# Optimization experiments

Measured on AMD Instinct MI355X. Metric: run time of the kernel, lower is better.

## Reference

```python
import jax, jax.numpy as jnp
import numpy as np

E = 256
H = 512
LN_EPS = 1e-5
NORM_EPS = 1e-12


def setup_inputs() -> dict:
    key = jax.random.key(0)
    ks = jax.random.split(key, 8)
    B, N, M = 8, 128, 128
    track_features = jax.random.normal(ks[0], (B, N, E), dtype=jnp.float32)
    det_features = jax.random.normal(ks[1], (B, M, E), dtype=jnp.float32)
    # MLP params (torch Linear default init style: uniform, but values irrelevant for correctness harness)
    lim1 = 1.0 / np.sqrt(3 * E)
    W1 = jax.random.uniform(ks[2], (3 * E, H), minval=-lim1, maxval=lim1, dtype=jnp.float32)
    b1 = jax.random.uniform(ks[3], (H,), minval=-lim1, maxval=lim1, dtype=jnp.float32)
    gamma = jnp.ones((H,), dtype=jnp.float32)
    beta = jnp.zeros((H,), dtype=jnp.float32)
    lim2 = 1.0 / np.sqrt(H)
    W2 = jax.random.uniform(ks[4], (H, 1), minval=-lim2, maxval=lim2, dtype=jnp.float32)
    b2 = jax.random.uniform(ks[5], (1,), minval=-lim2, maxval=lim2, dtype=jnp.float32)
    return {"track_features": track_features, "det_features": det_features,
            "W1": W1, "b1": b1, "gamma": gamma, "beta": beta, "W2": W2, "b2": b2}


def _l2_normalize(x):
    # F.normalize(x, dim=-1): x / max(||x||_2, eps)
    n = jnp.sqrt(jnp.sum(x * x, axis=-1, keepdims=True))
    return x / jnp.maximum(n, NORM_EPS)


def reference(track_features, det_features, W1, b1, gamma, beta, W2, b2):
    t = _l2_normalize(track_features)   # (B, N, E)
    d = _l2_normalize(det_features)     # (B, M, E)
    tb = t[:, :, None, :]               # (B, N, 1, E)
    db = d[:, None, :, :]               # (B, 1, M, E)
    B, N, _ = t.shape
    M = d.shape[1]
    diff = jnp.abs(tb - db)                                  # (B, N, M, E)
    pair = jnp.concatenate([jnp.broadcast_to(tb, (B, N, M, E)),
                            jnp.broadcast_to(db, (B, N, M, E)),
                            diff], axis=-1)                  # (B, N, M, 3E)
    h = jnp.einsum('bnme,eh->bnmh', pair, W1) + b1           # (B, N, M, H)
    mu = jnp.mean(h, axis=-1, keepdims=True)
    var = jnp.mean((h - mu) ** 2, axis=-1, keepdims=True)
    h = (h - mu) * jax.lax.rsqrt(var + LN_EPS) * gamma + beta
    h = h * jax.nn.sigmoid(h)                                # SiLU
    out = jnp.einsum('bnmh,ho->bnmo', h, W2)[..., 0] + b2[0]  # (B, N, M)
    return out
```

## Files before the change

kernel.cpp:

```cpp
#include <hip/hip_runtime.h>
#include <hip/hip_bf16.h>
#include <cstdint>

typedef __bf16 bf16x8 __attribute__((ext_vector_type(8)));
typedef float f32x4 __attribute__((ext_vector_type(4)));

#define E_DIM 256
#define H_DIM 512
#define TSTR 260

__global__ __launch_bounds__(256)
void w1conv_kernel(const float* __restrict__ W1, __bf16* __restrict__ W1cc) {
    int u = blockIdx.x * 256 + threadIdx.x;
    int j   = u & 3;
    int h   = (u >> 2) & 511;
    int c   = (u >> 11) & 7;
    int mat = u >> 14;
    bf16x8 v;
#pragma unroll
    for (int i = 0; i < 8; ++i)
        v[i] = (__bf16)W1[(size_t)(mat * 256 + c * 32 + j * 8 + i) * H_DIM + h];
    *(bf16x8*)(W1cc + ((size_t)(mat * 8 + c) * 512 + h) * 32 + j * 8) = v;
}

__global__ __launch_bounds__(512, 4)
void pq_mfma_kernel(const float* __restrict__ track, const float* __restrict__ det,
                    const __bf16* __restrict__ W1cc, const float* __restrict__ b1,
                    float* __restrict__ P, float* __restrict__ Q) {
    __shared__ __align__(16) __bf16 Ash[64 * 256];
    __shared__ float sclS[64];

    int tid  = threadIdx.x;
    int lane = tid & 63;
    int wave = tid >> 6;
    int lq   = lane >> 4;
    int lc   = lane & 15;

    int blk = blockIdx.x;
    bool isP = blk < 16;
    int r0 = (blk & 15) * 64;
    const float* src = isP ? track : det;

#pragma unroll
    for (int i = 0; i < 8; ++i) {
        int row = wave * 8 + i;
        float4 x = ((const float4*)(src + (size_t)(r0 + row) * E_DIM))[lane];
        float ss = x.x*x.x + x.y*x.y + x.z*x.z + x.w*x.w;
#pragma unroll
        for (int off = 32; off > 0; off >>= 1) ss += __shfl_xor(ss, off);
        if (lane == 0) sclS[row] = 1.0f / fmaxf(sqrtf(ss), 1e-12f);
    }
    __syncthreads();

#pragma unroll
    for (int r = 0; r < 4; ++r) {
        int row = r * 16 + lc;
        float st = sclS[row];
        const float* gp = src + (size_t)(r0 + row) * E_DIM + wave * 32 + lq * 8;
        float4 t0 = *(const float4*)gp;
        float4 t1 = *(const float4*)(gp + 4);
        bf16x8 v;
        v[0] = (__bf16)(t0.x * st); v[1] = (__bf16)(t0.y * st);
        v[2] = (__bf16)(t0.z * st); v[3] = (__bf16)(t0.w * st);
        v[4] = (__bf16)(t1.x * st); v[5] = (__bf16)(t1.y * st);
        v[6] = (__bf16)(t1.z * st); v[7] = (__bf16)(t1.w * st);
        *(bf16x8*)&Ash[(size_t)(r * 512 + wave * 64 + lane) * 8] = v;
    }
    __syncthreads();

    const uint4* Wg = (const uint4*)W1cc + (isP ? 0 : 16384);
    int hb = wave * 64 + lc;
    bf16x8 bwA[4], bwB[4];
#pragma unroll
    for (int ht = 0; ht < 4; ++ht)
        bwA[ht] = __builtin_bit_cast(bf16x8, Wg[(hb + ht * 16) * 4 + lq]);

    f32x4 acc[4][4];
#pragma unroll
    for (int pt = 0; pt < 4; ++pt)
#pragma unroll
        for (int ht = 0; ht < 4; ++ht)
            acc[pt][ht] = (f32x4){0.f, 0.f, 0.f, 0.f};

#pragma unroll
    for (int c = 0; c < 8; ++c) {
        bf16x8* cur = (c & 1) ? bwB : bwA;
        bf16x8* nxt = (c & 1) ? bwA : bwB;
        if (c < 7) {
#pragma unroll
            for (int ht = 0; ht < 4; ++ht)
                nxt[ht] = __builtin_bit_cast(bf16x8, Wg[(c + 1) * 2048 + (hb + ht * 16) * 4 + lq]);
        }
#pragma unroll
        for (int pt = 0; pt < 4; ++pt) {
            bf16x8 af = *(const bf16x8*)&Ash[(size_t)((pt * 8 + c) * 64 + lane) * 8];
#pragma unroll
            for (int ht = 0; ht < 4; ++ht)
                acc[pt][ht] = __builtin_amdgcn_mfma_f32_16x16x32_bf16(cur[ht], af, acc[pt][ht], 0, 0, 0);
        }
    }

    float* dst = isP ? P : Q;
#pragma unroll
    for (int ht = 0; ht < 4; ++ht) {
        int h = wave * 64 + ht * 16 + lq * 4;
        f32x4 bvv = (f32x4){0.f, 0.f, 0.f, 0.f};
        if (isP) bvv = *(const f32x4*)&b1[h];
#pragma unroll
        for (int pt = 0; pt < 4; ++pt) {
            f32x4 o = acc[pt][ht] + bvv;
            *(f32x4*)&dst[(size_t)(r0 + pt * 16 + lc) * H_DIM + h] = o;
        }
    }
}

__global__ __launch_bounds__(512, 4)
void main_kernel(const float* __restrict__ track, const float* __restrict__ det,
                 const __bf16* __restrict__ W1cc,
                 const float* __restrict__ P, const float* __restrict__ Q,
                 const float* __restrict__ gamma, const float* __restrict__ beta,
                 const float* __restrict__ W2, const float* __restrict__ b2,
                 float* __restrict__ out) {
    __shared__ __align__(16) char SMEM[49408];
    __bf16* Ash  = (__bf16*)SMEM;
    float*  tsl  = (float*)(SMEM + 32768);
    float*  dsl  = (float*)(SMEM + 41088);
    float*  LNr1 = (float*)(SMEM + 32768);
    float*  LNr2 = (float*)(SMEM + 35072);
    float*  Red2 = (float*)(SMEM + 37376);
    float*  MuS  = (float*)(SMEM + 39680);
    float*  RsS  = (float*)(SMEM + 39936);
    __shared__ float sclT[8], sclD[8];

    int tid  = threadIdx.x;
    int lane = tid & 63;
    int wave = tid >> 6;
    int lq   = lane >> 4;
    int lc   = lane & 15;

    int blk = blockIdx.x;
    int b   = blk >> 8;
    int n0  = ((blk >> 4) & 15) * 8;
    int m0  = (blk & 15) * 8;

    float4 tstage = ((const float4*)(track + (size_t)(b * 128 + n0 + wave) * E_DIM))[lane];
    float4 dstage = ((const float4*)(det   + (size_t)(b * 128 + m0 + wave) * E_DIM))[lane];

    const uint4* Wg = (const uint4*)W1cc + 32768;
    int hb = wave * 64 + lc;
    bf16x8 bwA[4], bwB[4];
#pragma unroll
    for (int ht = 0; ht < 4; ++ht)
        bwA[ht] = __builtin_bit_cast(bf16x8, Wg[(hb + ht * 16) * 4 + lq]);

    {
        float a = tstage.x*tstage.x + tstage.y*tstage.y + tstage.z*tstage.z + tstage.w*tstage.w;
        float d = dstage.x*dstage.x + dstage.y*dstage.y + dstage.z*dstage.z + dstage.w*dstage.w;
#pragma unroll
        for (int off = 32; off > 0; off >>= 1) { a += __shfl_xor(a, off); d += __shfl_xor(d, off); }
        if (lane == 0) {
            sclT[wave] = 1.0f / fmaxf(sqrtf(a), 1e-12f);
            sclD[wave] = 1.0f / fmaxf(sqrtf(d), 1e-12f);
        }
    }
    *(float4*)&tsl[wave * TSTR + lane * 4] = tstage;
    *(float4*)&dsl[wave * TSTR + lane * 4] = dstage;
    __syncthreads();

    {
        int k0 = wave * 32 + lq * 8;
        int ml = lane & 7;
        float sd = sclD[ml];
        const float* dr = dsl + ml * TSTR + k0;
        float4 d0 = *(const float4*)dr;
        float4 d1 = *(const float4*)(dr + 4);
#pragma unroll
        for (int r = 0; r < 4; ++r) {
            int nl = r * 2 + (lc >> 3);
            float st = sclT[nl];
            const float* tr = tsl + nl * TSTR + k0;
            float4 t0 = *(const float4*)tr;
            float4 t1 = *(const float4*)(tr + 4);
            bf16x8 v;
            v[0] = (__bf16)fabsf(t0.x * st - d0.x * sd);
            v[1] = (__bf16)fabsf(t0.y * st - d0.y * sd);
            v[2] = (__bf16)fabsf(t0.z * st - d0.z * sd);
            v[3] = (__bf16)fabsf(t0.w * st - d0.w * sd);
            v[4] = (__bf16)fabsf(t1.x * st - d1.x * sd);
            v[5] = (__bf16)fabsf(t1.y * st - d1.y * sd);
            v[6] = (__bf16)fabsf(t1.z * st - d1.z * sd);
            v[7] = (__bf16)fabsf(t1.w * st - d1.w * sd);
            *(bf16x8*)&Ash[(size_t)(r * 512 + wave * 64 + lane) * 8] = v;
        }
    }
    __syncthreads();

    f32x4 acc[4][4];
#pragma unroll
    for (int pt = 0; pt < 4; ++pt)
#pragma unroll
        for (int ht = 0; ht < 4; ++ht)
            acc[pt][ht] = (f32x4){0.f, 0.f, 0.f, 0.f};

#pragma unroll
    for (int c = 0; c < 8; ++c) {
        bf16x8* cur = (c & 1) ? bwB : bwA;
        bf16x8* nxt = (c & 1) ? bwA : bwB;
        if (c < 7) {
#pragma unroll
            for (int ht = 0; ht < 4; ++ht)
                nxt[ht] = __builtin_bit_cast(bf16x8, Wg[(c + 1) * 2048 + (hb + ht * 16) * 4 + lq]);
        }
#pragma unroll
        for (int pt = 0; pt < 4; ++pt) {
            bf16x8 af = *(const bf16x8*)&Ash[(size_t)((pt * 8 + c) * 64 + lane) * 8];
#pragma unroll
            for (int ht = 0; ht < 4; ++ht)
                acc[pt][ht] = __builtin_amdgcn_mfma_f32_16x16x32_bf16(cur[ht], af, acc[pt][ht], 0, 0, 0);
        }
    }

    const float* Pb = P + (size_t)(b * 128 + n0) * H_DIM;
    const float* Qb = Q + (size_t)(b * 128 + m0) * H_DIM;
    f32x4 qv[4];
#pragma unroll
    for (int ht = 0; ht < 4; ++ht)
        qv[ht] = *(const f32x4*)&Qb[(size_t)(lc & 7) * H_DIM + wave * 64 + ht * 16 + lq * 4];
#pragma unroll
    for (int pt = 0; pt < 4; ++pt) {
        int n = pt * 2 + (lc >> 3);
#pragma unroll
        for (int ht = 0; ht < 4; ++ht) {
            f32x4 pv = *(const f32x4*)&Pb[(size_t)n * H_DIM + wave * 64 + ht * 16 + lq * 4];
            acc[pt][ht] += pv + qv[ht];
        }
    }

#pragma unroll
    for (int pt = 0; pt < 4; ++pt) {
        float s1 = 0.f, s2 = 0.f;
#pragma unroll
        for (int ht = 0; ht < 4; ++ht)
#pragma unroll
            for (int rg = 0; rg < 4; ++rg) {
                float v = acc[pt][ht][rg];
                s1 += v; s2 += v * v;
            }
        s1 += __shfl_xor(s1, 16); s2 += __shfl_xor(s2, 16);
        s1 += __shfl_xor(s1, 32); s2 += __shfl_xor(s2, 32);
        if (lq == 0) {
            LNr1[(pt * 16 + lc) * 9 + wave] = s1;
            LNr2[(pt * 16 + lc) * 9 + wave] = s2;
        }
    }
    __syncthreads();
    if (tid < 64) {
        float S1 = 0.f, S2 = 0.f;
#pragma unroll
        for (int w = 0; w < 8; ++w) { S1 += LNr1[tid * 9 + w]; S2 += LNr2[tid * 9 + w]; }
        float mu = S1 * (1.0f / 512.0f);
        float var = S2 * (1.0f / 512.0f) - mu * mu;
        MuS[tid] = mu;
        RsS[tid] = rsqrtf(var + 1e-5f);
    }
    __syncthreads();

    f32x4 gvv[4], bvv[4], wvv[4];
#pragma unroll
    for (int ht = 0; ht < 4; ++ht) {
        int h = wave * 64 + ht * 16 + lq * 4;
        gvv[ht] = *(const f32x4*)&gamma[h];
        bvv[ht] = *(const f32x4*)&beta[h];
        wvv[ht] = *(const f32x4*)&W2[h];
    }
#pragma unroll
    for (int pt = 0; pt < 4; ++pt) {
        int pr = pt * 16 + lc;
        float mu = MuS[pr], rs = RsS[pr];
        float ca = 0.f;
#pragma unroll
        for (int ht = 0; ht < 4; ++ht)
#pragma unroll
            for (int rg = 0; rg < 4; ++rg) {
                float x = (acc[pt][ht][rg] - mu) * rs * gvv[ht][rg] + bvv[ht][rg];
                float sg = __builtin_amdgcn_rcpf(1.0f + __expf(-x));
                ca += x * sg * wvv[ht][rg];
            }
        ca += __shfl_xor(ca, 16);
        ca += __shfl_xor(ca, 32);
        if (lq == 0) Red2[pr * 9 + wave] = ca;
    }
    __syncthreads();
    if (tid < 64) {
        float o = b2[0];
#pragma unroll
        for (int w = 0; w < 8; ++w) o += Red2[tid * 9 + w];
        int n = n0 + (tid >> 3);
        int m = m0 + (tid & 7);
        out[(size_t)(b * 128 + n) * 128 + m] = o;
    }
}

extern "C" void kernel_launch(void* const* d_in, const int* in_sizes, int n_in,
                              void* d_out, int out_size, void* d_ws, size_t ws_size,
                              hipStream_t stream) {
    const float* track = (const float*)d_in[0];
    const float* det   = (const float*)d_in[1];
    const float* W1    = (const float*)d_in[2];
    const float* b1    = (const float*)d_in[3];
    const float* gamma = (const float*)d_in[4];
    const float* beta  = (const float*)d_in[5];
    const float* W2    = (const float*)d_in[6];
    const float* b2    = (const float*)d_in[7];
    float* out = (float*)d_out;

    char* ws = (char*)d_ws;
    float*  P     = (float*)(ws);
    float*  Q     = (float*)(ws + (2u << 20));
    __bf16* W1cc  = (__bf16*)(ws + (4u << 20));

    w1conv_kernel<<<192, 256, 0, stream>>>(W1, W1cc);
    pq_mfma_kernel<<<32, 512, 0, stream>>>(track, det, W1cc, b1, P, Q);
    main_kernel<<<2048, 512, 0, stream>>>(track, det, W1cc, P, Q, gamma, beta, W2, b2, out);
}
```

Before: 172.5 us.

## Split P/Q projection across H halves and reorder epilogue to cut registers

The P/Q precompute kernel now launches 64 blocks instead of 32, with each block computing half of the H dimension, so twice as many CUs run the small GEMM. Each block still normalizes its full 64-row tile, so that work is done twice. Separately, the main kernel's LayerNorm/SiLU epilogue is reordered to loop over ht on the outside and load gamma, beta and W2 per ht, which lowers live registers at the cost of four partial accumulators.

```diff
diff --git a/kernel.cpp b/kernel.cpp
--- a/kernel.cpp
+++ b/kernel.cpp
@@ -36,10 +36,13 @@
     int lq   = lane >> 4;
     int lc   = lane & 15;
 
-    int blk = blockIdx.x;
-    bool isP = blk < 16;
-    int r0 = (blk & 15) * 64;
-    const float* src = isP ? track : det;
+    int blk  = blockIdx.x;
+    int mat  = blk >> 5;
+    int rowg = (blk >> 1) & 15;
+    int half = blk & 1;
+    int r0   = rowg * 64;
+    int h0   = half * 256;
+    const float* src = mat ? det : track;
 
 #pragma unroll
     for (int i = 0; i < 8; ++i) {
@@ -68,18 +71,18 @@
     }
     __syncthreads();
 
-    const uint4* Wg = (const uint4*)W1cc + (isP ? 0 : 16384);
-    int hb = wave * 64 + lc;
-    bf16x8 bwA[4], bwB[4];
-#pragma unroll
-    for (int ht = 0; ht < 4; ++ht)
+    const uint4* Wg = (const uint4*)W1cc + (mat ? 16384 : 0);
+    int hb = h0 + wave * 32 + lc;
+    bf16x8 bwA[2], bwB[2];
+#pragma unroll
+    for (int ht = 0; ht < 2; ++ht)
         bwA[ht] = __builtin_bit_cast(bf16x8, Wg[(hb + ht * 16) * 4 + lq]);
 
-    f32x4 acc[4][4];
+    f32x4 acc[4][2];
 #pragma unroll
     for (int pt = 0; pt < 4; ++pt)
 #pragma unroll
-        for (int ht = 0; ht < 4; ++ht)
+        for (int ht = 0; ht < 2; ++ht)
             acc[pt][ht] = (f32x4){0.f, 0.f, 0.f, 0.f};
 
 #pragma unroll
@@ -88,24 +91,24 @@
         bf16x8* nxt = (c & 1) ? bwA : bwB;
         if (c < 7) {
 #pragma unroll
-            for (int ht = 0; ht < 4; ++ht)
+            for (int ht = 0; ht < 2; ++ht)
                 nxt[ht] = __builtin_bit_cast(bf16x8, Wg[(c + 1) * 2048 + (hb + ht * 16) * 4 + lq]);
         }
 #pragma unroll
         for (int pt = 0; pt < 4; ++pt) {
             bf16x8 af = *(const bf16x8*)&Ash[(size_t)((pt * 8 + c) * 64 + lane) * 8];
 #pragma unroll
-            for (int ht = 0; ht < 4; ++ht)
+            for (int ht = 0; ht < 2; ++ht)
                 acc[pt][ht] = __builtin_amdgcn_mfma_f32_16x16x32_bf16(cur[ht], af, acc[pt][ht], 0, 0, 0);
         }
     }
 
-    float* dst = isP ? P : Q;
-#pragma unroll
-    for (int ht = 0; ht < 4; ++ht) {
-        int h = wave * 64 + ht * 16 + lq * 4;
+    float* dst = mat ? Q : P;
+#pragma unroll
+    for (int ht = 0; ht < 2; ++ht) {
+        int h = h0 + wave * 32 + ht * 16 + lq * 4;
         f32x4 bvv = (f32x4){0.f, 0.f, 0.f, 0.f};
-        if (isP) bvv = *(const f32x4*)&b1[h];
+        if (!mat) bvv = *(const f32x4*)&b1[h];
 #pragma unroll
         for (int pt = 0; pt < 4; ++pt) {
             f32x4 o = acc[pt][ht] + bvv;
@@ -222,17 +225,19 @@
 
     const float* Pb = P + (size_t)(b * 128 + n0) * H_DIM;
     const float* Qb = Q + (size_t)(b * 128 + m0) * H_DIM;
-    f32x4 qv[4];
-#pragma unroll
-    for (int ht = 0; ht < 4; ++ht)
-        qv[ht] = *(const f32x4*)&Qb[(size_t)(lc & 7) * H_DIM + wave * 64 + ht * 16 + lq * 4];
-#pragma unroll
-    for (int pt = 0; pt < 4; ++pt) {
-        int n = pt * 2 + (lc >> 3);
-#pragma unroll
-        for (int ht = 0; ht < 4; ++ht) {
-            f32x4 pv = *(const f32x4*)&Pb[(size_t)n * H_DIM + wave * 64 + ht * 16 + lq * 4];
-            acc[pt][ht] += pv + qv[ht];
+    {
+        f32x4 qv[4];
+#pragma unroll
+        for (int ht = 0; ht < 4; ++ht)
+            qv[ht] = *(const f32x4*)&Qb[(size_t)(lc & 7) * H_DIM + wave * 64 + ht * 16 + lq * 4];
+#pragma unroll
+        for (int pt = 0; pt < 4; ++pt) {
+            int n = pt * 2 + (lc >> 3);
+#pragma unroll
+            for (int ht = 0; ht < 4; ++ht) {
+                f32x4 pv = *(const f32x4*)&Pb[(size_t)n * H_DIM + wave * 64 + ht * 16 + lq * 4];
+                acc[pt][ht] += pv + qv[ht];
+            }
         }
     }
 
@@ -265,30 +270,32 @@
     }
     __syncthreads();
 
-    f32x4 gvv[4], bvv[4], wvv[4];
+    float mus[4], rss[4];
+#pragma unroll
+    for (int pt = 0; pt < 4; ++pt) { mus[pt] = MuS[pt * 16 + lc]; rss[pt] = RsS[pt * 16 + lc]; }
+    float ca[4] = {0.f, 0.f, 0.f, 0.f};
 #pragma unroll
     for (int ht = 0; ht < 4; ++ht) {
         int h = wave * 64 + ht * 16 + lq * 4;
-        gvv[ht] = *(const f32x4*)&gamma[h];
-        bvv[ht] = *(const f32x4*)&beta[h];
-        wvv[ht] = *(const f32x4*)&W2[h];
+        f32x4 g = *(const f32x4*)&gamma[h];
+        f32x4 bb = *(const f32x4*)&beta[h];
+        f32x4 w = *(const f32x4*)&W2[h];
+#pragma unroll
+        for (int pt = 0; pt < 4; ++pt) {
+#pragma unroll
+            for (int rg = 0; rg < 4; ++rg) {
+                float x = (acc[pt][ht][rg] - mus[pt]) * rss[pt] * g[rg] + bb[rg];
+                float sg = __builtin_amdgcn_rcpf(1.0f + __expf(-x));
+                ca[pt] += x * sg * w[rg];
+            }
+        }
     }
 #pragma unroll
     for (int pt = 0; pt < 4; ++pt) {
-        int pr = pt * 16 + lc;
-        float mu = MuS[pr], rs = RsS[pr];
-        float ca = 0.f;
-#pragma unroll
-        for (int ht = 0; ht < 4; ++ht)
-#pragma unroll
-            for (int rg = 0; rg < 4; ++rg) {
-                float x = (acc[pt][ht][rg] - mu) * rs * gvv[ht][rg] + bvv[ht][rg];
-                float sg = __builtin_amdgcn_rcpf(1.0f + __expf(-x));
-                ca += x * sg * wvv[ht][rg];
-            }
-        ca += __shfl_xor(ca, 16);
-        ca += __shfl_xor(ca, 32);
-        if (lq == 0) Red2[pr * 9 + wave] = ca;
+        float c = ca[pt];
+        c += __shfl_xor(c, 16);
+        c += __shfl_xor(c, 32);
+        if (lq == 0) Red2[(pt * 16 + lc) * 9 + wave] = c;
     }
     __syncthreads();
     if (tid < 64) {
@@ -320,6 +327,6 @@
     __bf16* W1cc  = (__bf16*)(ws + (4u << 20));
 
     w1conv_kernel<<<192, 256, 0, stream>>>(W1, W1cc);
-    pq_mfma_kernel<<<32, 512, 0, stream>>>(track, det, W1cc, b1, P, Q);
+    pq_mfma_kernel<<<64, 512, 0, stream>>>(track, det, W1cc, b1, P, Q);
     main_kernel<<<2048, 512, 0, stream>>>(track, det, W1cc, P, Q, gamma, beta, W2, b2, out);
 }
```

New measurement: 163.9 us. 1.05x faster.
